# Optimization experiments

Measured on AMD Instinct MI355X. Metric: run time of the kernel, lower is better.

Reference implementation:

```python
import jax, jax.numpy as jnp
import numpy as np

N, D_IN, D_OUT = 8192, 128, 128

def setup_inputs() -> dict:
    key = jax.random.key(0)
    k1, k2, k3 = jax.random.split(key, 3)
    x = jax.random.normal(k1, (N, D_IN), dtype=jnp.float32)
    adjacency_matrix = jax.random.uniform(k2, (N, N), dtype=jnp.float32)
    weight = jax.random.normal(k3, (D_IN, D_OUT), dtype=jnp.float32) * (1.0 / np.sqrt(D_IN))
    return {"x": x, "adjacency_matrix": adjacency_matrix, "weight": weight}

def reference(x, adjacency_matrix, weight):
    # degree = row sums of A; D^{-1} A  ==  row-normalized adjacency.
    # (torch.inverse of the diagonal degree matrix is just 1/degree.)
    degree = jnp.sum(adjacency_matrix, axis=-1, keepdims=True)  # [N, 1]
    # Fuse: out = D^{-1} (A @ x) @ W  -- avoids materializing normalized A? 
    # Faithful math: (D^{-1} A) x W == D^{-1} (A x) W since D^{-1} is diagonal.
    ax = adjacency_matrix @ x                                   # [N, D_IN]
    out = (ax / degree) @ weight                                # [N, D_OUT]
    return out
```

## Files before the change

### kernel.cpp

```cpp
#include <hip/hip_runtime.h>
#include <hip/hip_bf16.h>

#define NN 8192
#define DD 128

typedef __attribute__((ext_vector_type(4))) float f32x4;
typedef __attribute__((ext_vector_type(16))) float f32x16;
typedef __attribute__((ext_vector_type(8))) short bf16x8;
typedef __attribute__((ext_vector_type(4))) short s16x4;

__device__ __forceinline__ short f2bf(float f) {
  __hip_bfloat16 h = __float2bfloat16(f);
  return __builtin_bit_cast(short, h);
}
__device__ __forceinline__ float bf2f(short s) {
  unsigned u = ((unsigned)(unsigned short)s) << 16;
  return __builtin_bit_cast(float, u);
}

template <int AUX>
__device__ __forceinline__ void async_copy16(void* lds, const void* g) {
  __builtin_amdgcn_global_load_lds(
      (const __attribute__((address_space(1))) void*)g,
      (__attribute__((address_space(3))) void*)lds, 16, 0, AUX);
}

__global__ __launch_bounds__(256) void xw_kernel(
    const float* __restrict__ x, const float* __restrict__ W,
    short* __restrict__ yT)
{
  __shared__ float xs[32][129];
  __shared__ float Ws[128 * 128];
  const int t  = threadIdx.x;
  const int k0 = blockIdx.x * 32;

  #pragma unroll
  for (int i = 0; i < 16; ++i) {
    int idx = (i * 256 + t) * 4;
    *(f32x4*)&Ws[idx] = *(const f32x4*)(W + idx);
  }
  #pragma unroll
  for (int i = 0; i < 4; ++i) {
    int idx = i * 256 + t;
    int row = idx >> 5;
    int c4  = (idx & 31) * 4;
    f32x4 v = *(const f32x4*)(x + (size_t)(k0 + row) * DD + c4);
    xs[row][c4 + 0] = v[0]; xs[row][c4 + 1] = v[1];
    xs[row][c4 + 2] = v[2]; xs[row][c4 + 3] = v[3];
  }
  __syncthreads();

  const int kl = t & 31;
  const int g  = t >> 5;
  float acc[16];
  #pragma unroll
  for (int j = 0; j < 16; ++j) acc[j] = 0.f;

  for (int d = 0; d < 128; ++d) {
    float xv = xs[kl][d];
    const float* wr = &Ws[d * 128 + g * 16];
    f32x4 w0 = *(const f32x4*)(wr);
    f32x4 w1 = *(const f32x4*)(wr + 4);
    f32x4 w2 = *(const f32x4*)(wr + 8);
    f32x4 w3 = *(const f32x4*)(wr + 12);
    #pragma unroll
    for (int j = 0; j < 4; ++j) {
      acc[j]      += xv * w0[j];
      acc[4 + j]  += xv * w1[j];
      acc[8 + j]  += xv * w2[j];
      acc[12 + j] += xv * w3[j];
    }
  }
  #pragma unroll
  for (int j = 0; j < 16; ++j) {
    int n = g * 16 + j;
    yT[(size_t)n * NN + k0 + kl] = f2bf(acc[j]);
  }
}

template <int ANT>
__device__ __forceinline__ void gcn_body(
    const float* __restrict__ A, const short* __restrict__ yT,
    short* __restrict__ part, float* __restrict__ degpart,
    float (&Abuf)[2][256 * 32], short (&Ybuf)[2][128 * 32])
{
  const int tid = threadIdx.x;
  const int l   = tid & 63;
  const int w   = tid >> 6;
  const int ks  = blockIdx.x & 7;
  const int mg  = blockIdx.x >> 3;
  const int R0  = mg * 256;
  const int kb  = ks * 1024;
  const int l31 = l & 31;
  const int hi  = l >> 5;
  const int wbase = w * 32;

  const int a_rin  = l >> 3;
  const int a_slot = l & 7;
  const float* gA[4];
  #pragma unroll
  for (int i = 0; i < 4; ++i) {
    const int r = wbase + 8 * i + a_rin;
    gA[i] = A + (size_t)(R0 + r) * NN + kb + ((a_slot ^ (r & 7)) << 2);
  }
  const int y_row = w * 16 + (l >> 2);
  const short* gY = yT + (size_t)y_row * NN + kb + (((l & 3) ^ (y_row & 3)) << 3);

  const int arx = l31 & 7;
  int aoff[2][2];
  #pragma unroll
  for (int j = 0; j < 2; ++j)
    #pragma unroll
    for (int q = 0; q < 2; ++q)
      aoff[j][q] = (wbase + l31) * 32 + (((4 * j + 2 * hi + q) ^ arx) << 2);
  int yoff[4][2];
  #pragma unroll
  for (int f = 0; f < 4; ++f)
    #pragma unroll
    for (int j = 0; j < 2; ++j)
      yoff[f][j] = (f * 32 + l31) * 32 + (((2 * j + hi) ^ (l31 & 3)) << 3);

  f32x16 acc[4];
  #pragma unroll
  for (int f = 0; f < 4; ++f) acc[f] = (f32x16)0.f;
  float deg = 0.f;

#define STAGE(buf, step) do {                                              \
    const int _k = (step) * 32;                                            \
    _Pragma("unroll")                                                      \
    for (int _i = 0; _i < 4; ++_i)                                         \
      async_copy16<ANT>(&Abuf[buf][(wbase + 8 * _i) * 32], gA[_i] + _k);   \
    async_copy16<0>(&Ybuf[buf][w * 512], gY + _k);                         \
  } while (0)

  STAGE(0, 0);
  STAGE(1, 1);

  for (int s = 0; s < 32; ++s) {
    __builtin_amdgcn_sched_barrier(0);
    if (s < 31) asm volatile("s_waitcnt vmcnt(5)" ::: "memory");
    else        asm volatile("s_waitcnt vmcnt(0)" ::: "memory");
    __builtin_amdgcn_sched_barrier(0);
    __builtin_amdgcn_s_barrier();
    __builtin_amdgcn_sched_barrier(0);

    const float* Ab = &Abuf[s & 1][0];
    const short* Yb = &Ybuf[s & 1][0];

    #pragma unroll
    for (int j = 0; j < 2; ++j) {
      f32x4 a0 = *(const f32x4*)&Ab[aoff[j][0]];
      f32x4 a1 = *(const f32x4*)&Ab[aoff[j][1]];

      deg += (a0[0] + a0[1]) + (a0[2] + a0[3])
           + (a1[0] + a1[1]) + (a1[2] + a1[3]);

      bf16x8 a;
      #pragma unroll
      for (int e = 0; e < 4; ++e) { a[e] = f2bf(a0[e]); a[4 + e] = f2bf(a1[e]); }

      #pragma unroll
      for (int f = 0; f < 4; ++f) {
        bf16x8 b = *(const bf16x8*)&Yb[yoff[f][j]];
        acc[f] = __builtin_amdgcn_mfma_f32_32x32x16_bf16(a, b, acc[f], 0, 0, 0);
      }
    }

    __builtin_amdgcn_sched_barrier(0);
    __builtin_amdgcn_s_barrier();
    __builtin_amdgcn_sched_barrier(0);
    if (s + 2 < 32) STAGE(s & 1, s + 2);
  }
#undef STAGE

  deg += __shfl_xor(deg, 32);
  if (l < 32)
    degpart[(size_t)ks * NN + R0 + wbase + l] = deg;

  short* pb = part + (size_t)ks * NN * DD + (size_t)(R0 + wbase) * DD;
  #pragma unroll
  for (int f = 0; f < 4; ++f)
    #pragma unroll
    for (int r = 0; r < 16; ++r) {
      const int row = (r & 3) + 8 * (r >> 2) + 4 * hi;
      __builtin_nontemporal_store(f2bf(acc[f][r]),
          pb + (size_t)row * DD + f * 32 + l31);
    }
}

__global__ __launch_bounds__(512, 4) void gcn_main(
    const float* __restrict__ A, const short* __restrict__ yT,
    short* __restrict__ part, float* __restrict__ degpart)
{
  __shared__ float Abuf[2][256 * 32];
  __shared__ short Ybuf[2][128 * 32];
  const int mg = blockIdx.x >> 3;
  if (mg & 1) gcn_body<2>(A, yT, part, degpart, Abuf, Ybuf);
  else        gcn_body<0>(A, yT, part, degpart, Abuf, Ybuf);
}

__global__ __launch_bounds__(256) void reduce_kernel(
    const short* __restrict__ part, const float* __restrict__ degpart,
    float* __restrict__ out)
{
  const int idx = blockIdx.x * 256 + threadIdx.x;
  const int m   = idx >> 5;
  const int c4  = (idx & 31) * 4;

  float s0 = 0.f, s1 = 0.f, s2 = 0.f, s3 = 0.f, d = 0.f;
  #pragma unroll
  for (int ks = 0; ks < 8; ++ks) {
    s16x4 v = *(const s16x4*)(part + (size_t)ks * NN * DD + (size_t)m * DD + c4);
    s0 += bf2f(v[0]); s1 += bf2f(v[1]); s2 += bf2f(v[2]); s3 += bf2f(v[3]);
    d += degpart[(size_t)ks * NN + m];
  }
  f32x4 r;
  r[0] = s0 / d; r[1] = s1 / d; r[2] = s2 / d; r[3] = s3 / d;
  *(f32x4*)(out + (size_t)m * DD + c4) = r;
}

extern "C" void kernel_launch(void* const* d_in, const int* in_sizes, int n_in,
                              void* d_out, int out_size, void* d_ws, size_t ws_size,
                              hipStream_t stream) {
  const float* x = (const float*)d_in[0];
  const float* A = (const float*)d_in[1];
  const float* W = (const float*)d_in[2];
  float* out = (float*)d_out;

  char* ws = (char*)d_ws;
  short* yT      = (short*)ws;
  short* part    = (short*)(ws + (2u << 20));
  float* degpart = (float*)(ws + (2u << 20) + (16u << 20));

  xw_kernel<<<256, 256, 0, stream>>>(x, W, yT);
  gcn_main<<<256, 512, 0, stream>>>(A, yT, part, degpart);
  reduce_kernel<<<1024, 256, 0, stream>>>(part, degpart, out);
}
```

Baseline: 85.43 us.

## Fuse split-K reduction into main GCN kernel via per-row-group atomic counters

```diff
diff --git a/kernel.cpp b/kernel.cpp
--- a/kernel.cpp
+++ b/kernel.cpp
@@ -7,7 +7,6 @@
 typedef __attribute__((ext_vector_type(4))) float f32x4;
 typedef __attribute__((ext_vector_type(16))) float f32x16;
 typedef __attribute__((ext_vector_type(8))) short bf16x8;
-typedef __attribute__((ext_vector_type(4))) short s16x4;
 
 __device__ __forceinline__ short f2bf(float f) {
   __hip_bfloat16 h = __float2bfloat16(f);
@@ -82,6 +81,7 @@
 __device__ __forceinline__ void gcn_body(
     const float* __restrict__ A, const short* __restrict__ yT,
     short* __restrict__ part, float* __restrict__ degpart,
+    float* __restrict__ out, unsigned* __restrict__ cnt,
     float (&Abuf)[2][256 * 32], short (&Ybuf)[2][128 * 32])
 {
   const int tid = threadIdx.x;
@@ -183,40 +183,52 @@
     #pragma unroll
     for (int r = 0; r < 16; ++r) {
       const int row = (r & 3) + 8 * (r >> 2) + 4 * hi;
-      __builtin_nontemporal_store(f2bf(acc[f][r]),
-          pb + (size_t)row * DD + f * 32 + l31);
+      pb[(size_t)row * DD + f * 32 + l31] = f2bf(acc[f][r]);
     }
+
+  __syncthreads();
+  if (tid == 0) {
+    __threadfence();
+    __hip_atomic_fetch_add(&cnt[mg], 1u, __ATOMIC_RELEASE,
+                           __HIP_MEMORY_SCOPE_AGENT);
+    while (__hip_atomic_load(&cnt[mg], __ATOMIC_ACQUIRE,
+                             __HIP_MEMORY_SCOPE_AGENT) < 8u)
+      __builtin_amdgcn_s_sleep(8);
+  }
+  __syncthreads();
+  __threadfence();
+
+  const int frow = R0 + ks * 32 + (tid >> 4);
+  const int fcol = (tid & 15) * 8;
+  float s8[8];
+  #pragma unroll
+  for (int e = 0; e < 8; ++e) s8[e] = 0.f;
+  float dsum = 0.f;
+  #pragma unroll
+  for (int q = 0; q < 8; ++q) {
+    bf16x8 v = *(const bf16x8*)(part + (size_t)q * NN * DD
+                                     + (size_t)frow * DD + fcol);
+    #pragma unroll
+    for (int e = 0; e < 8; ++e) s8[e] += bf2f(v[e]);
+    dsum += degpart[(size_t)q * NN + frow];
+  }
+  f32x4 o0, o1;
+  #pragma unroll
+  for (int e = 0; e < 4; ++e) { o0[e] = s8[e] / dsum; o1[e] = s8[4 + e] / dsum; }
+  *(f32x4*)(out + (size_t)frow * DD + fcol)     = o0;
+  *(f32x4*)(out + (size_t)frow * DD + fcol + 4) = o1;
 }
 
 __global__ __launch_bounds__(512, 4) void gcn_main(
     const float* __restrict__ A, const short* __restrict__ yT,
-    short* __restrict__ part, float* __restrict__ degpart)
+    short* __restrict__ part, float* __restrict__ degpart,
+    float* __restrict__ out, unsigned* __restrict__ cnt)
 {
   __shared__ float Abuf[2][256 * 32];
   __shared__ short Ybuf[2][128 * 32];
   const int mg = blockIdx.x >> 3;
-  if (mg & 1) gcn_body<2>(A, yT, part, degpart, Abuf, Ybuf);
-  else        gcn_body<0>(A, yT, part, degpart, Abuf, Ybuf);
-}
-
-__global__ __launch_bounds__(256) void reduce_kernel(
-    const short* __restrict__ part, const float* __restrict__ degpart,
-    float* __restrict__ out)
-{
-  const int idx = blockIdx.x * 256 + threadIdx.x;
-  const int m   = idx >> 5;
-  const int c4  = (idx & 31) * 4;
-
-  float s0 = 0.f, s1 = 0.f, s2 = 0.f, s3 = 0.f, d = 0.f;
-  #pragma unroll
-  for (int ks = 0; ks < 8; ++ks) {
-    s16x4 v = *(const s16x4*)(part + (size_t)ks * NN * DD + (size_t)m * DD + c4);
-    s0 += bf2f(v[0]); s1 += bf2f(v[1]); s2 += bf2f(v[2]); s3 += bf2f(v[3]);
-    d += degpart[(size_t)ks * NN + m];
-  }
-  f32x4 r;
-  r[0] = s0 / d; r[1] = s1 / d; r[2] = s2 / d; r[3] = s3 / d;
-  *(f32x4*)(out + (size_t)m * DD + c4) = r;
+  if (mg & 1) gcn_body<2>(A, yT, part, degpart, out, cnt, Abuf, Ybuf);
+  else        gcn_body<0>(A, yT, part, degpart, out, cnt, Abuf, Ybuf);
 }
 
 extern "C" void kernel_launch(void* const* d_in, const int* in_sizes, int n_in,
@@ -228,11 +240,12 @@
   float* out = (float*)d_out;
 
   char* ws = (char*)d_ws;
-  short* yT      = (short*)ws;
-  short* part    = (short*)(ws + (2u << 20));
-  float* degpart = (float*)(ws + (2u << 20) + (16u << 20));
-
+  short*    yT      = (short*)ws;
+  short*    part    = (short*)(ws + (2u << 20));
+  float*    degpart = (float*)(ws + (2u << 20) + (16u << 20));
+  unsigned* cnt     = (unsigned*)(ws + (2u << 20) + (16u << 20) + (256u << 10));
+
+  hipMemsetAsync(cnt, 0, 32 * sizeof(unsigned), stream);
   xw_kernel<<<256, 256, 0, stream>>>(x, W, yT);
-  gcn_main<<<256, 512, 0, stream>>>(A, yT, part, degpart);
-  reduce_kernel<<<1024, 256, 0, stream>>>(part, degpart, out);
-}
+  gcn_main<<<256, 512, 0, stream>>>(A, yT, part, degpart, out, cnt);
+}
```

Measured after the change: 171.5 us. 101% more time.
